# Optimization experiments

Hardware: AMD Instinct MI355X
Metric: run time of the kernel (lower is better)

The kernel has to match this reference:

```python
import jax, jax.numpy as jnp
import numpy as np
import math

B, S, D = 2, 2048, 1024
H, DK, DV = 16, 64, 64  # head_count, query_size, value_size; H*DV == D
NEG_INF = -jnp.inf


def setup_inputs() -> dict:
    key = jax.random.key(0)
    ks = jax.random.split(key, 10)
    sc = 0.02
    return {
        "input": jax.random.normal(ks[0], (B, S, D), dtype=jnp.float32),
        "padding_mask": jnp.zeros((B, S), dtype=jnp.float32),  # 0 = valid, 1 = padded
        "wq_w": jax.random.normal(ks[1], (H * DK, D), dtype=jnp.float32) * sc,
        "wq_b": jnp.zeros((H * DK,), dtype=jnp.float32),
        "wk_w": jax.random.normal(ks[2], (H * DK, D), dtype=jnp.float32) * sc,
        "wk_b": jnp.zeros((H * DK,), dtype=jnp.float32),
        "wv_w": jax.random.normal(ks[3], (H * DV, D), dtype=jnp.float32) * sc,
        "wv_b": jnp.zeros((H * DV,), dtype=jnp.float32),
        "fin_w": jax.random.normal(ks[4], (D, H * DV), dtype=jnp.float32) * sc,
        "fin_b": jnp.zeros((D,), dtype=jnp.float32),
    }


def reference(input, padding_mask, wq_w, wq_b, wk_w, wk_b, wv_w, wv_b, fin_w, fin_b):
    b, s, _ = input.shape
    # projections -> [b, h, s, d]
    Q = (input @ wq_w.T + wq_b).reshape(b, s, H, DK).transpose(0, 2, 1, 3)
    K = (input @ wk_w.T + wk_b).reshape(b, s, H, DK).transpose(0, 2, 1, 3)
    V = (input @ wv_w.T + wv_b).reshape(b, s, H, DV).transpose(0, 2, 1, 3)

    # padding mask: pad*(-inf), nan_to_num(0*inf -> 0); broadcast over query dim
    pad = jnp.where(padding_mask > 0, NEG_INF, 0.0)[:, None, None, :]  # [b,1,1,s]
    i = jnp.arange(s)
    causal = jnp.where(i[None, :] < i[:, None] + 1, 0.0, NEG_INF)  # [s,s]
    mask = pad + causal[None, None, :, :]

    # (QK^T + mask) / sqrt(dk), softmax over keys
    logits = (jnp.einsum("bhqd,bhkd->bhqk", Q, K) + mask) / math.sqrt(DK)
    attn = jax.nn.softmax(logits, axis=-1)
    out = jnp.einsum("bhqk,bhkd->bqhd", attn, V).reshape(b, s, H * DV)
    return out @ fin_w.T + fin_b
```

## Files before the change

kernel.cpp:

```cpp
#include <hip/hip_runtime.h>


typedef __bf16 bf16;
typedef __bf16 bf16x4 __attribute__((ext_vector_type(4)));
typedef __bf16 bf16x8 __attribute__((ext_vector_type(8)));
typedef float  f32x4  __attribute__((ext_vector_type(4)));

#define B_  2
#define S_  2048
#define D_  1024
#define H_  16
#define HD  64
#define NEG_BIG (-3.0e38f)
#define SCALE_LOG2E 0.1803368801111204f

#define NSPLIT_QT 14
#define SLOTS_PER_BH (2 * NSPLIT_QT)

__device__ __forceinline__ void lds16(const void* g, void* l) {
    __builtin_amdgcn_global_load_lds((const __attribute__((address_space(1))) void*)g,
                                     (__attribute__((address_space(3))) void*)l, 16, 0, 0);
}

__device__ __forceinline__ f32x4 mfma16(bf16x8 a, bf16x8 b, f32x4 c) {
    return __builtin_amdgcn_mfma_f32_16x16x32_bf16(a, b, c, 0, 0, 0);
}

#define IT(qt, k0, ke) ((uint32_t)(qt) | ((uint32_t)(k0) << 8) | ((uint32_t)(ke) << 16))
__device__ __constant__ uint32_t g_items[46] = {
    IT(16,0,9),  IT(17,0,9),
    IT(30,0,8),  IT(30,8,16), IT(31,0,8),  IT(31,8,16),
    IT(28,0,8),  IT(29,0,8),  IT(14,0,8),  IT(15,0,8),
    IT(28,8,15), IT(29,8,15), IT(26,0,7),  IT(26,7,14),
    IT(27,0,7),  IT(27,7,14), IT(24,0,7),  IT(25,0,7),
    IT(12,0,7),  IT(13,0,7),
    IT(24,7,13), IT(25,7,13), IT(22,0,6),  IT(22,6,12),
    IT(23,0,6),  IT(23,6,12), IT(20,0,6),  IT(21,0,6),
    IT(10,0,6),  IT(11,0,6),
    IT(20,6,11), IT(21,6,11), IT(18,0,5),  IT(18,5,10),
    IT(19,0,5),  IT(19,5,10), IT(8,0,5),   IT(9,0,5),
    IT(6,0,4),   IT(7,0,4),
    IT(4,0,3),   IT(5,0,3),
    IT(2,0,2),   IT(3,0,2),
    IT(0,0,1),   IT(1,0,1)
};

__global__ __launch_bounds__(256) void convert_k(const float* __restrict__ X,
                                                 const float* __restrict__ wq,
                                                 const float* __restrict__ wk,
                                                 const float* __restrict__ wv,
                                                 const float* __restrict__ wo,
                                                 const float* __restrict__ pm,
                                                 bf16* __restrict__ dst,
                                                 bf16* __restrict__ validB) {
    const int gid = blockIdx.x * 256 + threadIdx.x;
    const int i   = gid * 4;
    const float* src;
    int off;
    if      (i < (4 << 20)) { src = X;  off = 0; }
    else if (i < (5 << 20)) { src = wq; off = 4 << 20; }
    else if (i < (6 << 20)) { src = wk; off = 5 << 20; }
    else if (i < (7 << 20)) { src = wv; off = 6 << 20; }
    else                    { src = wo; off = 7 << 20; }
    const float4 v = *(const float4*)(src + (i - off));
    bf16x4 p;
    p[0] = (bf16)v.x; p[1] = (bf16)v.y; p[2] = (bf16)v.z; p[3] = (bf16)v.w;
    *(bf16x4*)(dst + i) = p;
    if (gid < (B_ * S_) / 4) {
        const float4 m = *(const float4*)(pm + gid * 4);
        bf16x4 q;
        q[0] = (bf16)((m.x > 0.f) ? 0.f : 1.f);
        q[1] = (bf16)((m.y > 0.f) ? 0.f : 1.f);
        q[2] = (bf16)((m.z > 0.f) ? 0.f : 1.f);
        q[3] = (bf16)((m.w > 0.f) ? 0.f : 1.f);
        *(bf16x4*)(validB + gid * 4) = q;
    }
}

__global__ __launch_bounds__(256) void gemm_qkv(const bf16* __restrict__ A,
                                                const bf16* __restrict__ Wq,
                                                const bf16* __restrict__ Wk,
                                                const bf16* __restrict__ Wv,
                                                const float* __restrict__ bq,
                                                const float* __restrict__ bk,
                                                const float* __restrict__ bv,
                                                const float* __restrict__ pm,
                                                bf16* __restrict__ Qw,
                                                bf16* __restrict__ Kw,
                                                bf16* __restrict__ Vw) {
    constexpr int K = 1024;
    __shared__ bf16 sA[2][128 * 32];
    __shared__ bf16 sB[2][128 * 32];
    const int tid  = threadIdx.x;
    const int l15  = tid & 15;
    const int quad = (tid & 63) >> 4;
    const int wid  = tid >> 6;
    const int seg  = blockIdx.x >> 3;
    const int bn   = blockIdx.x & 7;
    const int bm   = blockIdx.y;
    const int wm   = (wid >> 1) * 64;
    const int wn   = (wid & 1) * 64;

    const bf16* W    = (seg == 0) ? Wq : (seg == 1) ? Wk : Wv;
    const float* bias = (seg == 0) ? bq : (seg == 1) ? bk : bv;

    const bf16* Ab = A + (size_t)bm * 128 * K;
    const bf16* Wb = W + (size_t)bn * 128 * K;

    f32x4 acc[4][4] = {};
    const int rq = (quad ^ ((l15 >> 1) & 3)) * 8;

#define QSTAGE(BUF, K0) do {                                                    \
    _Pragma("unroll")                                                           \
    for (int it_ = 0; it_ < 2; ++it_) {                                         \
        int c_ = it_ * 256 + tid;                                               \
        int row_ = c_ >> 2, c8_ = c_ & 3;                                       \
        int sw_ = c8_ ^ ((row_ >> 1) & 3);                                      \
        lds16(Ab + row_ * K + (K0) + sw_ * 8, (char*)sA[BUF] + c_ * 16);        \
        lds16(Wb + row_ * K + (K0) + sw_ * 8, (char*)sB[BUF] + c_ * 16);        \
    } } while (0)

    QSTAGE(0, 0);
    __syncthreads();
    int cur = 0;
    for (int k0 = 0; k0 < K; k0 += 32) {
        if (k0 + 32 < K) QSTAGE(cur ^ 1, k0 + 32);
        bf16x8 af[4], bfr[4];
        #pragma unroll
        for (int i = 0; i < 4; ++i)
            af[i] = *(const bf16x8*)&sA[cur][(wm + i * 16 + l15) * 32 + rq];
        #pragma unroll
        for (int i = 0; i < 4; ++i)
            bfr[i] = *(const bf16x8*)&sB[cur][(wn + i * 16 + l15) * 32 + rq];
        #pragma unroll
        for (int mi = 0; mi < 4; ++mi)
            #pragma unroll
            for (int ni = 0; ni < 4; ++ni)
                acc[mi][ni] = mfma16(af[mi], bfr[ni], acc[mi][ni]);
        __syncthreads();
        cur ^= 1;
    }
#undef QSTAGE

    #pragma unroll
    for (int ni = 0; ni < 4; ++ni) {
        const int n  = bn * 128 + wn + ni * 16 + l15;
        const float bv_ = bias[n];
        const int h = n >> 6;
        #pragma unroll
        for (int mi = 0; mi < 4; ++mi) {
            const int m0 = bm * 128 + wm + mi * 16 + quad * 4;
            if (seg == 2) {
                const int dv = n & 63;
                const int b = m0 >> 11, s = m0 & 2047;
                const float4 pmv = *(const float4*)&pm[b * S_ + s];
                bf16x4 pack;
                #pragma unroll
                for (int r = 0; r < 4; ++r) {
                    const float vm = (((const float*)&pmv)[r] > 0.f) ? 0.f : 1.f;
                    pack[r] = (bf16)((acc[mi][ni][r] + bv_) * vm);
                }
                *(bf16x4*)&Vw[(((size_t)(b * H_ + h) * HD + dv) << 11) + s] = pack;
            } else {
                bf16* C = (seg == 0) ? Qw : Kw;
                const float qs = (seg == 0) ? SCALE_LOG2E : 1.0f;
                const int dk = n & 63;
                #pragma unroll
                for (int r = 0; r < 4; ++r) {
                    const int m = m0 + r, b = m >> 11, s = m & 2047;
                    C[(((size_t)(b * H_ + h) << 11) + s) * HD + dk] =
                        (bf16)((acc[mi][ni][r] + bv_) * qs);
                }
            }
        }
    }
}

__global__ __launch_bounds__(256) void gemm_fin(const bf16* __restrict__ A,
                                                const bf16* __restrict__ W,
                                                const float* __restrict__ bias,
                                                float* __restrict__ C) {
    constexpr int N = 1024, K = 1024;
    __shared__ bf16 sA[2][64 * 32];
    __shared__ bf16 sB[2][128 * 32];
    const int tid  = threadIdx.x;
    const int l15  = tid & 15;
    const int quad = (tid & 63) >> 4;
    const int wid  = tid >> 6;
    const int bm   = blockIdx.x >> 3;
    const int bn   = blockIdx.x & 7;
    const int wm   = (wid & 1) * 32;
    const int wn   = (wid >> 1) * 64;

    const bf16* Ab = A + (size_t)bm * 64 * K;
    const bf16* Wb = W + (size_t)bn * 128 * K;

    f32x4 acc[2][4] = {};
    const int rq = (quad ^ ((l15 >> 1) & 3)) * 8;

#define FSTAGE(BUF, K0) do {                                                    \
    {   int c_ = tid;                                                           \
        int row_ = c_ >> 2, c8_ = c_ & 3;                                       \
        int sw_ = c8_ ^ ((row_ >> 1) & 3);                                      \
        lds16(Ab + row_ * K + (K0) + sw_ * 8, (char*)sA[BUF] + c_ * 16); }      \
    _Pragma("unroll")                                                           \
    for (int it_ = 0; it_ < 2; ++it_) {                                         \
        int c_ = it_ * 256 + tid;                                               \
        int row_ = c_ >> 2, c8_ = c_ & 3;                                       \
        int sw_ = c8_ ^ ((row_ >> 1) & 3);                                      \
        lds16(Wb + row_ * K + (K0) + sw_ * 8, (char*)sB[BUF] + c_ * 16);        \
    } } while (0)

    FSTAGE(0, 0);
    __syncthreads();
    int cur = 0;
    for (int k0 = 0; k0 < K; k0 += 32) {
        if (k0 + 32 < K) FSTAGE(cur ^ 1, k0 + 32);
        bf16x8 af[2], bfr[4];
        #pragma unroll
        for (int i = 0; i < 2; ++i)
            af[i] = *(const bf16x8*)&sA[cur][(wm + i * 16 + l15) * 32 + rq];
        #pragma unroll
        for (int i = 0; i < 4; ++i)
            bfr[i] = *(const bf16x8*)&sB[cur][(wn + i * 16 + l15) * 32 + rq];
        #pragma unroll
        for (int mi = 0; mi < 2; ++mi)
            #pragma unroll
            for (int ni = 0; ni < 4; ++ni)
                acc[mi][ni] = mfma16(af[mi], bfr[ni], acc[mi][ni]);
        __syncthreads();
        cur ^= 1;
    }
#undef FSTAGE

    #pragma unroll
    for (int ni = 0; ni < 4; ++ni) {
        const int n  = bn * 128 + wn + ni * 16 + l15;
        const float bv = bias[n];
        #pragma unroll
        for (int mi = 0; mi < 2; ++mi) {
            const int m0 = bm * 64 + wm + mi * 16 + quad * 4;
            #pragma unroll
            for (int r = 0; r < 4; ++r)
                C[(size_t)(m0 + r) * N + n] = acc[mi][ni][r] + bv;
        }
    }
}

__global__ __launch_bounds__(256, 4) void attn_k(const bf16* __restrict__ Q,
                                                 const bf16* __restrict__ K,
                                                 const bf16* __restrict__ Vt,
                                                 const bf16* __restrict__ validB,
                                                 float* __restrict__ Opart,
                                                 float* __restrict__ Lpart,
                                                 bf16* __restrict__ Aout) {
    __shared__ bf16 sK_[2 * 128 * 32];
    __shared__ bf16 sV[4 * 64 * 32];
    const int tid  = threadIdx.x;
    const int l15  = tid & 15;
    const int quad = (tid & 63) >> 4;
    const int wid  = tid >> 6;
    const int bh   = blockIdx.x & 31;
    const int b    = bh >> 4;
    const int h    = bh & 15;

    const uint32_t itm = g_items[blockIdx.x >> 5];
    const int qt  = itm & 255;
    const int kt0 = (itm >> 8) & 255;
    const int kte = (itm >> 16) & 255;
    const int nkt = (qt >> 1) + 1;
    const bool split = (qt >= 18);

    const bf16* Qg = Q  + (size_t)bh * S_ * HD;
    const bf16* Kg = K  + (size_t)bh * S_ * HD;
    const bf16* Vg = Vt + (size_t)bh * HD * S_;
    const bf16* vB = validB + b * S_;

    bf16x8 qb[2];
    #pragma unroll
    for (int kk = 0; kk < 2; ++kk)
        qb[kk] = *(const bf16x8*)&Qg[(qt * 64 + wid * 16 + l15) * HD + kk * 32 + quad * 8];

    const int krow0 = (l15 >> 2) * 8 + (l15 & 3);
    const int qg    = qt * 64 + wid * 16 + l15;
    const int ckx = (quad ^ (((l15 >> 1) & 1) | (((l15 >> 2) & 1) << 1))) * 8;
    const int cvx = (quad ^ (((l15 >> 1) & 1) | (((l15 >> 3) & 1) << 1))) * 8;

    f32x4 o[4]  = {};
    f32x4 lacc  = {};

    for (int kt = kt0; kt < kte; ++kt) {
        __syncthreads();
        #pragma unroll
        for (int it = 0; it < 4; ++it) {
            int c = it * 256 + tid;
            { int pl = c >> 9, row = (c >> 2) & 127, c8 = c & 3;
              int sw = c8 ^ (((row >> 1) & 1) | (((row >> 3) & 1) << 1));
              lds16(Kg + ((size_t)kt * 128 + row) * HD + pl * 32 + sw * 8,
                    (char*)sK_ + c * 16); }
            { int kc = c >> 8, dv = (c >> 2) & 63, c8 = c & 3;
              int sw = c8 ^ (((dv >> 1) & 1) | (((dv >> 3) & 1) << 1));
              lds16(Vg + (size_t)kt * 128 + (size_t)dv * S_ + kc * 32 + sw * 8,
                    (char*)sV + c * 16); }
        }
        bf16x8 vf[4];
        #pragma unroll
        for (int g = 0; g < 4; ++g)
            vf[g] = *(const bf16x8*)&vB[kt * 128 + g * 32 + quad * 8];
        __syncthreads();

        const bool lastt = (kt == nkt - 1);
        #pragma unroll
        for (int g = 0; g < 4; ++g) {
            f32x4 s[2] = {};
            #pragma unroll
            for (int f = 0; f < 2; ++f)
                #pragma unroll
                for (int kk = 0; kk < 2; ++kk) {
                    bf16x8 ka = *(const bf16x8*)
                        &sK_[(kk * 128 + g * 32 + krow0 + f * 4) * 32 + ckx];
                    s[f] = mfma16(ka, qb[kk], s[f]);
                }
            bf16x8 pb;
            #pragma unroll
            for (int f = 0; f < 2; ++f)
                #pragma unroll
                for (int r = 0; r < 4; ++r) {
                    float v = s[f][r];
                    if (lastt && (kt * 128 + g * 32 + quad * 8 + f * 4 + r > qg))
                        v = NEG_BIG;
                    pb[f * 4 + r] = (bf16)exp2f(v);
                }
            lacc = mfma16(vf[g], pb, lacc);
            #pragma unroll
            for (int dvf = 0; dvf < 4; ++dvf) {
                bf16x8 va = *(const bf16x8*)
                    &sV[(g * 64 + dvf * 16 + l15) * 32 + cvx];
                o[dvf] = mfma16(va, pb, o[dvf]);
            }
        }
    }

    if (split) {
        const int sidx = (qt - 18) * 2 + (kt0 ? 1 : 0);
        const int slot = bh * SLOTS_PER_BH + sidx;
        const int q    = wid * 16 + l15;
        float* Ob = Opart + ((size_t)slot << 12) + q * 64 + quad * 4;
        #pragma unroll
        for (int dvf = 0; dvf < 4; ++dvf)
            *(f32x4*)(Ob + dvf * 16) = o[dvf];
        if (quad == 0) Lpart[slot * 64 + q] = lacc[0];
    } else {
        const float inv = 1.f / lacc[0];
        const size_t base = ((size_t)b * S_ + qg) * D_ + h * HD + quad * 4;
        #pragma unroll
        for (int dvf = 0; dvf < 4; ++dvf) {
            bf16x4 pk;
            #pragma unroll
            for (int r = 0; r < 4; ++r) pk[r] = (bf16)(o[dvf][r] * inv);
            *(bf16x4*)&Aout[base + dvf * 16] = pk;
        }
    }
}

__global__ __launch_bounds__(256) void combine_k(const float* __restrict__ Opart,
                                                 const float* __restrict__ Lpart,
                                                 bf16* __restrict__ Aw) {
    const int gid  = blockIdx.x * 256 + threadIdx.x;
    const int dc   = gid & 7;
    const int q    = (gid >> 3) & 63;
    const int rest = gid >> 9;
    const int qth  = rest % NSPLIT_QT;
    const int bh   = rest / NSPLIT_QT;
    const int slot0 = bh * SLOTS_PER_BH + qth * 2;
    const float l = Lpart[slot0 * 64 + q] + Lpart[(slot0 + 1) * 64 + q];
    const float inv = 1.f / l;
    const float* O0 = Opart + ((size_t)slot0 << 12) + q * 64 + dc * 8;
    const float* O1 = O0 + 4096;
    const float4 a0 = *(const float4*)O0;
    const float4 a1 = *(const float4*)(O0 + 4);
    const float4 b0 = *(const float4*)O1;
    const float4 b1 = *(const float4*)(O1 + 4);
    bf16x8 p;
    p[0] = (bf16)((a0.x + b0.x) * inv); p[1] = (bf16)((a0.y + b0.y) * inv);
    p[2] = (bf16)((a0.z + b0.z) * inv); p[3] = (bf16)((a0.w + b0.w) * inv);
    p[4] = (bf16)((a1.x + b1.x) * inv); p[5] = (bf16)((a1.y + b1.y) * inv);
    p[6] = (bf16)((a1.z + b1.z) * inv); p[7] = (bf16)((a1.w + b1.w) * inv);
    const int b = bh >> 4, h = bh & 15;
    const int s = (18 + qth) * 64 + q;
    *(bf16x8*)&Aw[((size_t)(b * S_ + s)) * D_ + h * HD + dc * 8] = p;
}

extern "C" void kernel_launch(void* const* d_in, const int* in_sizes, int n_in,
                              void* d_out, int out_size, void* d_ws, size_t ws_size,
                              hipStream_t stream) {
    const float* X   = (const float*)d_in[0];
    const float* pm  = (const float*)d_in[1];
    const float* wq  = (const float*)d_in[2];
    const float* bq  = (const float*)d_in[3];
    const float* wk  = (const float*)d_in[4];
    const float* bk  = (const float*)d_in[5];
    const float* wv  = (const float*)d_in[6];
    const float* bvb = (const float*)d_in[7];
    const float* wo  = (const float*)d_in[8];
    const float* bo  = (const float*)d_in[9];
    float* out = (float*)d_out;

    char* ws = (char*)d_ws;
    bf16* Xb  = (bf16*)(ws);
    bf16* Wqb = (bf16*)(ws + (8u  << 20));
    bf16* Wkb = (bf16*)(ws + (10u << 20));
    bf16* Wvb = (bf16*)(ws + (12u << 20));
    bf16* Wob = (bf16*)(ws + (14u << 20));
    bf16* Qw  = (bf16*)(ws + (16u << 20));
    bf16* Kw  = (bf16*)(ws + (24u << 20));
    bf16* Vw  = (bf16*)(ws + (32u << 20));
    bf16* Aw  = (bf16*)(ws + (40u << 20));
    float* Opart = (float*)(ws);
    bf16*  validB = (bf16*)(ws + (48u << 20));
    float* Lpart  = (float*)(ws + (48u << 20) + 65536);

    convert_k<<<dim3(8192), dim3(256), 0, stream>>>(X, wq, wk, wv, wo, pm,
                                                    Xb, validB);
    gemm_qkv<<<dim3(24, 32), dim3(256), 0, stream>>>(Xb, Wqb, Wkb, Wvb,
                                                     bq, bk, bvb, pm,
                                                     Qw, Kw, Vw);
    attn_k<<<dim3(1472), dim3(256), 0, stream>>>(Qw, Kw, Vw, validB,
                                                 Opart, Lpart, Aw);
    combine_k<<<dim3(896), dim3(256), 0, stream>>>(Opart, Lpart, Aw);
    gemm_fin<<<dim3(512), dim3(256), 0, stream>>>(Aw, Wob, bo, out);
}
```

Measured before the change: 197.9 us.

## Replace split-K attention and combine kernel with paired causal tile scheduling

Removes the KV-split work list and the separate combine kernel, so each attention block now handles one full 64-row query tile. Tiles are ordered long-to-short in an interleaved pattern for rough load balance across 1024 blocks. This drops the partial-output round trip through global memory and one kernel launch. The cost is a worse critical path, since the longest tiles now run unsplit. The convert kernel also switches to 8 elements per thread with 16-byte bf16 stores.

```diff
diff --git a/kernel.cpp b/kernel.cpp
--- a/kernel.cpp
+++ b/kernel.cpp
@@ -14,9 +14,6 @@
 #define NEG_BIG (-3.0e38f)
 #define SCALE_LOG2E 0.1803368801111204f
 
-#define NSPLIT_QT 14
-#define SLOTS_PER_BH (2 * NSPLIT_QT)
-
 __device__ __forceinline__ void lds16(const void* g, void* l) {
     __builtin_amdgcn_global_load_lds((const __attribute__((address_space(1))) void*)g,
                                      (__attribute__((address_space(3))) void*)l, 16, 0, 0);
@@ -26,24 +23,12 @@
     return __builtin_amdgcn_mfma_f32_16x16x32_bf16(a, b, c, 0, 0, 0);
 }
 
-#define IT(qt, k0, ke) ((uint32_t)(qt) | ((uint32_t)(k0) << 8) | ((uint32_t)(ke) << 16))
-__device__ __constant__ uint32_t g_items[46] = {
-    IT(16,0,9),  IT(17,0,9),
-    IT(30,0,8),  IT(30,8,16), IT(31,0,8),  IT(31,8,16),
-    IT(28,0,8),  IT(29,0,8),  IT(14,0,8),  IT(15,0,8),
-    IT(28,8,15), IT(29,8,15), IT(26,0,7),  IT(26,7,14),
-    IT(27,0,7),  IT(27,7,14), IT(24,0,7),  IT(25,0,7),
-    IT(12,0,7),  IT(13,0,7),
-    IT(24,7,13), IT(25,7,13), IT(22,0,6),  IT(22,6,12),
-    IT(23,0,6),  IT(23,6,12), IT(20,0,6),  IT(21,0,6),
-    IT(10,0,6),  IT(11,0,6),
-    IT(20,6,11), IT(21,6,11), IT(18,0,5),  IT(18,5,10),
-    IT(19,0,5),  IT(19,5,10), IT(8,0,5),   IT(9,0,5),
-    IT(6,0,4),   IT(7,0,4),
-    IT(4,0,3),   IT(5,0,3),
-    IT(2,0,2),   IT(3,0,2),
-    IT(0,0,1),   IT(1,0,1)
-};
+__device__ __forceinline__ bf16x8 cvt8(const float4 a, const float4 b) {
+    bf16x8 v;
+    v[0] = (bf16)a.x; v[1] = (bf16)a.y; v[2] = (bf16)a.z; v[3] = (bf16)a.w;
+    v[4] = (bf16)b.x; v[5] = (bf16)b.y; v[6] = (bf16)b.z; v[7] = (bf16)b.w;
+    return v;
+}
 
 __global__ __launch_bounds__(256) void convert_k(const float* __restrict__ X,
                                                  const float* __restrict__ wq,
@@ -54,7 +39,7 @@
                                                  bf16* __restrict__ dst,
                                                  bf16* __restrict__ validB) {
     const int gid = blockIdx.x * 256 + threadIdx.x;
-    const int i   = gid * 4;
+    const int i   = gid * 8;
     const float* src;
     int off;
     if      (i < (4 << 20)) { src = X;  off = 0; }
@@ -62,18 +47,22 @@
     else if (i < (6 << 20)) { src = wk; off = 5 << 20; }
     else if (i < (7 << 20)) { src = wv; off = 6 << 20; }
     else                    { src = wo; off = 7 << 20; }
-    const float4 v = *(const float4*)(src + (i - off));
-    bf16x4 p;
-    p[0] = (bf16)v.x; p[1] = (bf16)v.y; p[2] = (bf16)v.z; p[3] = (bf16)v.w;
-    *(bf16x4*)(dst + i) = p;
-    if (gid < (B_ * S_) / 4) {
-        const float4 m = *(const float4*)(pm + gid * 4);
-        bf16x4 q;
-        q[0] = (bf16)((m.x > 0.f) ? 0.f : 1.f);
-        q[1] = (bf16)((m.y > 0.f) ? 0.f : 1.f);
-        q[2] = (bf16)((m.z > 0.f) ? 0.f : 1.f);
-        q[3] = (bf16)((m.w > 0.f) ? 0.f : 1.f);
-        *(bf16x4*)(validB + gid * 4) = q;
+    const float4 v0 = *(const float4*)(src + (i - off));
+    const float4 v1 = *(const float4*)(src + (i - off) + 4);
+    *(bf16x8*)(dst + i) = cvt8(v0, v1);
+    if (gid < (B_ * S_) / 8) {
+        const float4 m0 = *(const float4*)(pm + gid * 8);
+        const float4 m1 = *(const float4*)(pm + gid * 8 + 4);
+        bf16x8 q;
+        q[0] = (bf16)((m0.x > 0.f) ? 0.f : 1.f);
+        q[1] = (bf16)((m0.y > 0.f) ? 0.f : 1.f);
+        q[2] = (bf16)((m0.z > 0.f) ? 0.f : 1.f);
+        q[3] = (bf16)((m0.w > 0.f) ? 0.f : 1.f);
+        q[4] = (bf16)((m1.x > 0.f) ? 0.f : 1.f);
+        q[5] = (bf16)((m1.y > 0.f) ? 0.f : 1.f);
+        q[6] = (bf16)((m1.z > 0.f) ? 0.f : 1.f);
+        q[7] = (bf16)((m1.w > 0.f) ? 0.f : 1.f);
+        *(bf16x8*)(validB + gid * 8) = q;
     }
 }
 
@@ -176,6 +165,107 @@
     }
 }
 
+__global__ __launch_bounds__(256, 4) void attn_k(const bf16* __restrict__ Q,
+                                                 const bf16* __restrict__ K,
+                                                 const bf16* __restrict__ Vt,
+                                                 const bf16* __restrict__ validB,
+                                                 bf16* __restrict__ Aout) {
+    __shared__ bf16 sK_[2 * 128 * 32];
+    __shared__ bf16 sV[4 * 64 * 32];
+    const int tid  = threadIdx.x;
+    const int l15  = tid & 15;
+    const int quad = (tid & 63) >> 4;
+    const int wid  = tid >> 6;
+    const int j    = blockIdx.x >> 5;
+    const int bh   = blockIdx.x & 31;
+    const int b    = bh >> 4;
+    const int h    = bh & 15;
+    const int a_  = j >> 3, bq_ = j & 7;
+    const int qt  = (a_ == 0) ? (31 - bq_) : (a_ == 1) ? bq_
+                  : (a_ == 2) ? (23 - bq_) : (8 + bq_);
+    const int nkt = (qt >> 1) + 1;
+
+    const bf16* Qg = Q  + (size_t)bh * S_ * HD;
+    const bf16* Kg = K  + (size_t)bh * S_ * HD;
+    const bf16* Vg = Vt + (size_t)bh * HD * S_;
+    const bf16* vB = validB + b * S_;
+
+    bf16x8 qb[2];
+    #pragma unroll
+    for (int kk = 0; kk < 2; ++kk)
+        qb[kk] = *(const bf16x8*)&Qg[(qt * 64 + wid * 16 + l15) * HD + kk * 32 + quad * 8];
+
+    const int krow0 = (l15 >> 2) * 8 + (l15 & 3);
+    const int qg    = qt * 64 + wid * 16 + l15;
+    const int ckx = (quad ^ (((l15 >> 1) & 1) | (((l15 >> 2) & 1) << 1))) * 8;
+    const int cvx = (quad ^ (((l15 >> 1) & 1) | (((l15 >> 3) & 1) << 1))) * 8;
+
+    f32x4 o[4]  = {};
+    f32x4 lacc  = {};
+
+    for (int kt = 0; kt < nkt; ++kt) {
+        __syncthreads();
+        #pragma unroll
+        for (int it = 0; it < 4; ++it) {
+            int c = it * 256 + tid;
+            { int pl = c >> 9, row = (c >> 2) & 127, c8 = c & 3;
+              int sw = c8 ^ (((row >> 1) & 1) | (((row >> 3) & 1) << 1));
+              lds16(Kg + ((size_t)kt * 128 + row) * HD + pl * 32 + sw * 8,
+                    (char*)sK_ + c * 16); }
+            { int kc = c >> 8, dv = (c >> 2) & 63, c8 = c & 3;
+              int sw = c8 ^ (((dv >> 1) & 1) | (((dv >> 3) & 1) << 1));
+              lds16(Vg + (size_t)kt * 128 + (size_t)dv * S_ + kc * 32 + sw * 8,
+                    (char*)sV + c * 16); }
+        }
+        bf16x8 vf[4];
+        #pragma unroll
+        for (int g = 0; g < 4; ++g)
+            vf[g] = *(const bf16x8*)&vB[kt * 128 + g * 32 + quad * 8];
+        __syncthreads();
+
+        const bool lastt = (kt == nkt - 1);
+        #pragma unroll
+        for (int g = 0; g < 4; ++g) {
+            f32x4 s[2] = {};
+            #pragma unroll
+            for (int f = 0; f < 2; ++f)
+                #pragma unroll
+                for (int kk = 0; kk < 2; ++kk) {
+                    bf16x8 ka = *(const bf16x8*)
+                        &sK_[(kk * 128 + g * 32 + krow0 + f * 4) * 32 + ckx];
+                    s[f] = mfma16(ka, qb[kk], s[f]);
+                }
+            bf16x8 pb;
+            #pragma unroll
+            for (int f = 0; f < 2; ++f)
+                #pragma unroll
+                for (int r = 0; r < 4; ++r) {
+                    float v = s[f][r];
+                    if (lastt && (kt * 128 + g * 32 + quad * 8 + f * 4 + r > qg))
+                        v = NEG_BIG;
+                    pb[f * 4 + r] = (bf16)exp2f(v);
+                }
+            lacc = mfma16(vf[g], pb, lacc);
+            #pragma unroll
+            for (int dvf = 0; dvf < 4; ++dvf) {
+                bf16x8 va = *(const bf16x8*)
+                    &sV[(g * 64 + dvf * 16 + l15) * 32 + cvx];
+                o[dvf] = mfma16(va, pb, o[dvf]);
+            }
+        }
+    }
+
+    const float inv = 1.f / lacc[0];
+    const size_t base = ((size_t)b * S_ + qg) * D_ + h * HD + quad * 4;
+    #pragma unroll
+    for (int dvf = 0; dvf < 4; ++dvf) {
+        bf16x4 pk;
+        #pragma unroll
+        for (int r = 0; r < 4; ++r) pk[r] = (bf16)(o[dvf][r] * inv);
+        *(bf16x4*)&Aout[base + dvf * 16] = pk;
+    }
+}
+
 __global__ __launch_bounds__(256) void gemm_fin(const bf16* __restrict__ A,
                                                 const bf16* __restrict__ W,
                                                 const float* __restrict__ bias,
@@ -247,150 +337,6 @@
     }
 }
 
-__global__ __launch_bounds__(256, 4) void attn_k(const bf16* __restrict__ Q,
-                                                 const bf16* __restrict__ K,
-                                                 const bf16* __restrict__ Vt,
-                                                 const bf16* __restrict__ validB,
-                                                 float* __restrict__ Opart,
-                                                 float* __restrict__ Lpart,
-                                                 bf16* __restrict__ Aout) {
-    __shared__ bf16 sK_[2 * 128 * 32];
-    __shared__ bf16 sV[4 * 64 * 32];
-    const int tid  = threadIdx.x;
-    const int l15  = tid & 15;
-    const int quad = (tid & 63) >> 4;
-    const int wid  = tid >> 6;
-    const int bh   = blockIdx.x & 31;
-    const int b    = bh >> 4;
-    const int h    = bh & 15;
-
-    const uint32_t itm = g_items[blockIdx.x >> 5];
-    const int qt  = itm & 255;
-    const int kt0 = (itm >> 8) & 255;
-    const int kte = (itm >> 16) & 255;
-    const int nkt = (qt >> 1) + 1;
-    const bool split = (qt >= 18);
-
-    const bf16* Qg = Q  + (size_t)bh * S_ * HD;
-    const bf16* Kg = K  + (size_t)bh * S_ * HD;
-    const bf16* Vg = Vt + (size_t)bh * HD * S_;
-    const bf16* vB = validB + b * S_;
-
-    bf16x8 qb[2];
-    #pragma unroll
-    for (int kk = 0; kk < 2; ++kk)
-        qb[kk] = *(const bf16x8*)&Qg[(qt * 64 + wid * 16 + l15) * HD + kk * 32 + quad * 8];
-
-    const int krow0 = (l15 >> 2) * 8 + (l15 & 3);
-    const int qg    = qt * 64 + wid * 16 + l15;
-    const int ckx = (quad ^ (((l15 >> 1) & 1) | (((l15 >> 2) & 1) << 1))) * 8;
-    const int cvx = (quad ^ (((l15 >> 1) & 1) | (((l15 >> 3) & 1) << 1))) * 8;
-
-    f32x4 o[4]  = {};
-    f32x4 lacc  = {};
-
-    for (int kt = kt0; kt < kte; ++kt) {
-        __syncthreads();
-        #pragma unroll
-        for (int it = 0; it < 4; ++it) {
-            int c = it * 256 + tid;
-            { int pl = c >> 9, row = (c >> 2) & 127, c8 = c & 3;
-              int sw = c8 ^ (((row >> 1) & 1) | (((row >> 3) & 1) << 1));
-              lds16(Kg + ((size_t)kt * 128 + row) * HD + pl * 32 + sw * 8,
-                    (char*)sK_ + c * 16); }
-            { int kc = c >> 8, dv = (c >> 2) & 63, c8 = c & 3;
-              int sw = c8 ^ (((dv >> 1) & 1) | (((dv >> 3) & 1) << 1));
-              lds16(Vg + (size_t)kt * 128 + (size_t)dv * S_ + kc * 32 + sw * 8,
-                    (char*)sV + c * 16); }
-        }
-        bf16x8 vf[4];
-        #pragma unroll
-        for (int g = 0; g < 4; ++g)
-            vf[g] = *(const bf16x8*)&vB[kt * 128 + g * 32 + quad * 8];
-        __syncthreads();
-
-        const bool lastt = (kt == nkt - 1);
-        #pragma unroll
-        for (int g = 0; g < 4; ++g) {
-            f32x4 s[2] = {};
-            #pragma unroll
-            for (int f = 0; f < 2; ++f)
-                #pragma unroll
-                for (int kk = 0; kk < 2; ++kk) {
-                    bf16x8 ka = *(const bf16x8*)
-                        &sK_[(kk * 128 + g * 32 + krow0 + f * 4) * 32 + ckx];
-                    s[f] = mfma16(ka, qb[kk], s[f]);
-                }
-            bf16x8 pb;
-            #pragma unroll
-            for (int f = 0; f < 2; ++f)
-                #pragma unroll
-                for (int r = 0; r < 4; ++r) {
-                    float v = s[f][r];
-                    if (lastt && (kt * 128 + g * 32 + quad * 8 + f * 4 + r > qg))
-                        v = NEG_BIG;
-                    pb[f * 4 + r] = (bf16)exp2f(v);
-                }
-            lacc = mfma16(vf[g], pb, lacc);
-            #pragma unroll
-            for (int dvf = 0; dvf < 4; ++dvf) {
-                bf16x8 va = *(const bf16x8*)
-                    &sV[(g * 64 + dvf * 16 + l15) * 32 + cvx];
-                o[dvf] = mfma16(va, pb, o[dvf]);
-            }
-        }
-    }
-
-    if (split) {
-        const int sidx = (qt - 18) * 2 + (kt0 ? 1 : 0);
-        const int slot = bh * SLOTS_PER_BH + sidx;
-        const int q    = wid * 16 + l15;
-        float* Ob = Opart + ((size_t)slot << 12) + q * 64 + quad * 4;
-        #pragma unroll
-        for (int dvf = 0; dvf < 4; ++dvf)
-            *(f32x4*)(Ob + dvf * 16) = o[dvf];
-        if (quad == 0) Lpart[slot * 64 + q] = lacc[0];
-    } else {
-        const float inv = 1.f / lacc[0];
-        const size_t base = ((size_t)b * S_ + qg) * D_ + h * HD + quad * 4;
-        #pragma unroll
-        for (int dvf = 0; dvf < 4; ++dvf) {
-            bf16x4 pk;
-            #pragma unroll
-            for (int r = 0; r < 4; ++r) pk[r] = (bf16)(o[dvf][r] * inv);
-            *(bf16x4*)&Aout[base + dvf * 16] = pk;
-        }
-    }
-}
-
-__global__ __launch_bounds__(256) void combine_k(const float* __restrict__ Opart,
-                                                 const float* __restrict__ Lpart,
-                                                 bf16* __restrict__ Aw) {
-    const int gid  = blockIdx.x * 256 + threadIdx.x;
-    const int dc   = gid & 7;
-    const int q    = (gid >> 3) & 63;
-    const int rest = gid >> 9;
-    const int qth  = rest % NSPLIT_QT;
-    const int bh   = rest / NSPLIT_QT;
-    const int slot0 = bh * SLOTS_PER_BH + qth * 2;
-    const float l = Lpart[slot0 * 64 + q] + Lpart[(slot0 + 1) * 64 + q];
-    const float inv = 1.f / l;
-    const float* O0 = Opart + ((size_t)slot0 << 12) + q * 64 + dc * 8;
-    const float* O1 = O0 + 4096;
-    const float4 a0 = *(const float4*)O0;
-    const float4 a1 = *(const float4*)(O0 + 4);
-    const float4 b0 = *(const float4*)O1;
-    const float4 b1 = *(const float4*)(O1 + 4);
-    bf16x8 p;
-    p[0] = (bf16)((a0.x + b0.x) * inv); p[1] = (bf16)((a0.y + b0.y) * inv);
-    p[2] = (bf16)((a0.z + b0.z) * inv); p[3] = (bf16)((a0.w + b0.w) * inv);
-    p[4] = (bf16)((a1.x + b1.x) * inv); p[5] = (bf16)((a1.y + b1.y) * inv);
-    p[6] = (bf16)((a1.z + b1.z) * inv); p[7] = (bf16)((a1.w + b1.w) * inv);
-    const int b = bh >> 4, h = bh & 15;
-    const int s = (18 + qth) * 64 + q;
-    *(bf16x8*)&Aw[((size_t)(b * S_ + s)) * D_ + h * HD + dc * 8] = p;
-}
-
 extern "C" void kernel_launch(void* const* d_in, const int* in_sizes, int n_in,
                               void* d_out, int out_size, void* d_ws, size_t ws_size,
                               hipStream_t stream) {
@@ -416,17 +362,13 @@
     bf16* Kw  = (bf16*)(ws + (24u << 20));
     bf16* Vw  = (bf16*)(ws + (32u << 20));
     bf16* Aw  = (bf16*)(ws + (40u << 20));
-    float* Opart = (float*)(ws);
-    bf16*  validB = (bf16*)(ws + (48u << 20));
-    float* Lpart  = (float*)(ws + (48u << 20) + 65536);
-
-    convert_k<<<dim3(8192), dim3(256), 0, stream>>>(X, wq, wk, wv, wo, pm,
+    bf16* validB = (bf16*)(ws + (48u << 20));
+
+    convert_k<<<dim3(4096), dim3(256), 0, stream>>>(X, wq, wk, wv, wo, pm,
                                                     Xb, validB);
     gemm_qkv<<<dim3(24, 32), dim3(256), 0, stream>>>(Xb, Wqb, Wkb, Wvb,
                                                      bq, bk, bvb, pm,
                                                      Qw, Kw, Vw);
-    attn_k<<<dim3(1472), dim3(256), 0, stream>>>(Qw, Kw, Vw, validB,
-                                                 Opart, Lpart, Aw);
-    combine_k<<<dim3(896), dim3(256), 0, stream>>>(Opart, Lpart, Aw);
+    attn_k<<<dim3(1024), dim3(256), 0, stream>>>(Qw, Kw, Vw, validB, Aw);
     gemm_fin<<<dim3(512), dim3(256), 0, stream>>>(Aw, Wob, bo, out);
 }
```

New measurement: 191.8 us. 3.1% less time.
